# Kernel optimization log

Measured on AMD Instinct MI355X. Metric: run time of the kernel, lower is better.

## Reference

```python
import jax, jax.numpy as jnp
import numpy as np

N, TO, TI, H = 8, 2048, 2048, 128
MASK_FILL = -99999.0  # module uses -99999.0, not -inf


def setup_inputs() -> dict:
    key = jax.random.key(0)
    kq, kv, km = jax.random.split(key, 3)
    queries = jax.random.normal(kq, (N, TO, H), dtype=jnp.float32)
    values = jax.random.normal(kv, (N, TI, H), dtype=jnp.float32)
    # mask is applied to scores.view(-1, Ti) -> shape (N*To, Ti), True = masked
    mask = jax.random.randint(km, (N * TO, TI), 0, 2).astype(bool)
    return {"queries": queries, "values": values, "mask": mask}


def reference(queries, values, mask):
    n, to, h = queries.shape
    ti = values.shape[1]
    # N x To x Ti scores (no 1/sqrt(H) scaling in the original)
    scores = jnp.einsum("nth,nsh->nts", queries, values)
    scores = jnp.where(mask.reshape(n, to, ti), MASK_FILL, scores)
    attention_distribution = jax.nn.softmax(scores, axis=-1)
    attention_output = jnp.einsum("nts,nsh->nth", attention_distribution, values)
    return attention_output, attention_distribution
```

## Files before the change

### kernel.cpp

```cpp
#include <hip/hip_runtime.h>

#define NB  8
#define TOQ 2048
#define TIV 2048
#define HD  128

typedef float f32x4 __attribute__((ext_vector_type(4)));
typedef short s16x8 __attribute__((ext_vector_type(8)));
typedef unsigned short ushort4v __attribute__((ext_vector_type(4)));
typedef unsigned short ushort8v __attribute__((ext_vector_type(8)));

__device__ __forceinline__ unsigned short f2bf(float f) {
    unsigned u = __float_as_uint(f);
    return (unsigned short)((u + 0x7FFFu + ((u >> 16) & 1u)) >> 16);
}
__device__ __forceinline__ float bf2f(unsigned short h) {
    return __uint_as_float(((unsigned)h) << 16);
}

__device__ __forceinline__ void split8(const float4 a, const float4 b,
                                       ushort8v& h, ushort8v& l) {
    const float x[8] = {a.x, a.y, a.z, a.w, b.x, b.y, b.z, b.w};
    #pragma unroll
    for (int j = 0; j < 8; ++j) {
        const unsigned short hi = f2bf(x[j]);
        h[j] = hi;
        l[j] = f2bf(x[j] - bf2f(hi));
    }
}

__device__ __forceinline__ void gload16(const void* g, void* l) {
    __builtin_amdgcn_global_load_lds(
        (const __attribute__((address_space(1))) void*)g,
        (__attribute__((address_space(3))) void*)l, 16, 0, 0);
}

__global__ __launch_bounds__(256) void k0_split(
    const float* __restrict__ Q, const float* __restrict__ V,
    unsigned short* __restrict__ Qh, unsigned short* __restrict__ Ql,
    unsigned short* __restrict__ Vh, unsigned short* __restrict__ Vl)
{
    const size_t i = ((size_t)blockIdx.x * 256 + threadIdx.x) * 8;
    const float* src = blockIdx.y ? V : Q;
    unsigned short* dh = blockIdx.y ? Vh : Qh;
    unsigned short* dl = blockIdx.y ? Vl : Ql;
    const float4 a = *(const float4*)&src[i];
    const float4 b = *(const float4*)&src[i + 4];
    ushort8v h, l;
    split8(a, b, h, l);
    *(ushort8v*)&dh[i] = h;
    *(ushort8v*)&dl[i] = l;
}

__global__ __launch_bounds__(256) void k0_vtf(
    const float* __restrict__ V, unsigned short* __restrict__ VTf)
{
    __shared__ unsigned short tile[64][68];
    const int n  = blockIdx.z;
    const int s0 = blockIdx.x * 64;
    const int h0 = blockIdx.y * 64;
    const int t  = threadIdx.x;

    #pragma unroll
    for (int it = 0; it < 4; ++it) {
        const int f = t + it * 256;
        const int r = f >> 4;
        const int c = f & 15;
        const float4 v = *(const float4*)&V[((size_t)(n * TIV + s0 + r)) * HD + h0 + 4 * c];
        tile[4 * c + 0][r] = f2bf(v.x);
        tile[4 * c + 1][r] = f2bf(v.y);
        tile[4 * c + 2][r] = f2bf(v.z);
        tile[4 * c + 3][r] = f2bf(v.w);
    }
    __syncthreads();

    #pragma unroll
    for (int it = 0; it < 2; ++it) {
        const int s    = t * 2 + it;
        const int k32i = s >> 8;
        const int fni  = (s >> 6) & 3;
        const int l    = s & 63;
        const int hh   = fni * 16 + (l & 15);
        const int kloc = k32i * 32 + ((l >> 4) * 8);
        ushort8v o;
        #pragma unroll
        for (int j = 0; j < 8; ++j) o[j] = tile[hh][kloc + j];
        const size_t k32g = (size_t)(s0 >> 5) + k32i;
        const size_t fng  = (size_t)(h0 >> 4) + fni;
        *(ushort8v*)&VTf[(((size_t)n * 64 + k32g) * 8 + fng) * 512 + (size_t)l * 8] = o;
    }
}

__global__ __launch_bounds__(256) void k0_vt_old(
    const float* __restrict__ V, unsigned short* __restrict__ VT)
{
    __shared__ unsigned short tile[64][68];
    const int n  = blockIdx.z;
    const int s0 = blockIdx.x * 64;
    const int h0 = blockIdx.y * 64;
    const int t  = threadIdx.x;

    #pragma unroll
    for (int it = 0; it < 4; ++it) {
        const int f = t + it * 256;
        const int r = f >> 4;
        const int c = f & 15;
        const float4 v = *(const float4*)&V[((size_t)(n * TIV + s0 + r)) * HD + h0 + 4 * c];
        tile[4 * c + 0][r] = f2bf(v.x);
        tile[4 * c + 1][r] = f2bf(v.y);
        tile[4 * c + 2][r] = f2bf(v.z);
        tile[4 * c + 3][r] = f2bf(v.w);
    }
    __syncthreads();

    #pragma unroll
    for (int it = 0; it < 2; ++it) {
        const int f  = t + it * 256;
        const int hh = f >> 3;
        const int sc = f & 7;
        ushort8v o;
        #pragma unroll
        for (int j = 0; j < 8; ++j) o[j] = tile[hh][8 * sc + j];
        *(ushort8v*)&VT[((size_t)(n * HD + h0 + hh)) * TIV + s0 + 8 * sc] = o;
    }
}

__global__ __launch_bounds__(512) void k1_w8(
    const unsigned short* __restrict__ QhG, const unsigned short* __restrict__ QlG,
    const unsigned short* __restrict__ VhG, const unsigned short* __restrict__ VlG,
    const int* __restrict__ M, unsigned short* __restrict__ Eb,
    float* __restrict__ part)
{
    __shared__ unsigned short qh_l[128 * 32], ql_l[128 * 32];
    __shared__ unsigned short vh_l[128 * 32], vl_l[128 * 32];

    const int n    = blockIdx.z;
    const int tt   = blockIdx.y * 128;
    const int ts   = blockIdx.x * 128;
    const int t    = threadIdx.x;
    const int lane = t & 63;
    const int wave = t >> 6;
    const int wr   = wave >> 2;
    const int wc   = wave & 3;
    const int lr   = lane & 15;
    const int kg   = lane >> 4;

    f32x4 acc[4][2];
    #pragma unroll
    for (int i = 0; i < 4; ++i)
        #pragma unroll
        for (int j = 0; j < 2; ++j) acc[i][j] = (f32x4)0.f;

    for (int h0 = 0; h0 < HD; h0 += 32) {
        {
            const int c   = wave * 64 + lane;
            const int row = c >> 2;
            const int kb  = (c & 3) * 8;
            const int lb  = wave * 512;
            const size_t qo = ((size_t)(n * TOQ + tt + row)) * HD + h0 + kb;
            const size_t vo = ((size_t)(n * TIV + ts + row)) * HD + h0 + kb;
            gload16(QhG + qo, qh_l + lb);
            gload16(QlG + qo, ql_l + lb);
            gload16(VhG + vo, vh_l + lb);
            gload16(VlG + vo, vl_l + lb);
        }
        __syncthreads();

        s16x8 aH[4], aL[4];
        #pragma unroll
        for (int fm = 0; fm < 4; ++fm) {
            const int off = (wr * 64 + fm * 16 + lr) * 32 + kg * 8;
            aH[fm] = *(const s16x8*)(vh_l + off);
            aL[fm] = *(const s16x8*)(vl_l + off);
        }
        #pragma unroll
        for (int fn = 0; fn < 2; ++fn) {
            const int off = (wc * 32 + fn * 16 + lr) * 32 + kg * 8;
            const s16x8 bH = *(const s16x8*)(qh_l + off);
            const s16x8 bL = *(const s16x8*)(ql_l + off);
            #pragma unroll
            for (int fm = 0; fm < 4; ++fm) {
                acc[fm][fn] = __builtin_amdgcn_mfma_f32_16x16x32_bf16(aH[fm], bH, acc[fm][fn], 0, 0, 0);
                acc[fm][fn] = __builtin_amdgcn_mfma_f32_16x16x32_bf16(aH[fm], bL, acc[fm][fn], 0, 0, 0);
                acc[fm][fn] = __builtin_amdgcn_mfma_f32_16x16x32_bf16(aL[fm], bH, acc[fm][fn], 0, 0, 0);
            }
        }
        __syncthreads();
    }

    #pragma unroll
    for (int fn = 0; fn < 2; ++fn) {
        const int to_g = tt + wc * 32 + fn * 16 + lr;
        const size_t rowbase = ((size_t)n * TOQ + to_g) * TIV;
        float rs = 0.f;
        #pragma unroll
        for (int fm = 0; fm < 4; ++fm) {
            const int ti_g = ts + wr * 64 + fm * 16 + kg * 4;
            const int4 mv = *(const int4*)&M[rowbase + ti_g];
            float4 e;
            e.x = mv.x ? 0.f : __expf(acc[fm][fn][0]);
            e.y = mv.y ? 0.f : __expf(acc[fm][fn][1]);
            e.z = mv.z ? 0.f : __expf(acc[fm][fn][2]);
            e.w = mv.w ? 0.f : __expf(acc[fm][fn][3]);
            ushort4v eb;
            eb[0] = f2bf(e.x); eb[1] = f2bf(e.y);
            eb[2] = f2bf(e.z); eb[3] = f2bf(e.w);
            *(ushort4v*)&Eb[rowbase + ti_g] = eb;
            rs += (e.x + e.y) + (e.z + e.w);
        }
        rs += __shfl_xor(rs, 16, 64);
        rs += __shfl_xor(rs, 32, 64);
        if (kg == 0)
            part[((size_t)n * TOQ + to_g) * 32 + blockIdx.x * 2 + wr] = rs;
    }
}

__global__ __launch_bounds__(256) void k1_reg(
    const float* __restrict__ Q, const float* __restrict__ V,
    const int* __restrict__ M, float* __restrict__ E,
    float* __restrict__ part)
{
    __shared__ unsigned short qhi[128 * 32], qlo[128 * 32];
    __shared__ unsigned short vhi[128 * 32], vlo[128 * 32];

    const int n    = blockIdx.z;
    const int tt   = blockIdx.y * 128;
    const int ts   = blockIdx.x * 128;
    const int t    = threadIdx.x;
    const int lane = t & 63;
    const int wave = t >> 6;
    const int wr   = wave >> 1;
    const int wc   = wave & 1;
    const int lr   = lane & 15;
    const int kg   = lane >> 4;

    const float* Qb = Q + ((size_t)n * TOQ + tt) * HD;
    const float* Vb = V + ((size_t)n * TIV + ts) * HD;

    f32x4 acc[4][4];
    #pragma unroll
    for (int i = 0; i < 4; ++i)
        #pragma unroll
        for (int j = 0; j < 4; ++j) acc[i][j] = (f32x4)0.f;

    for (int h0 = 0; h0 < HD; h0 += 32) {
        #pragma unroll
        for (int it = 0; it < 2; ++it) {
            const int i   = t + it * 256;
            const int row = i >> 2;
            const int kb  = i & 3;
            const float* qs = Qb + (size_t)row * HD + h0 + kb * 8;
            const float* vs = Vb + (size_t)row * HD + h0 + kb * 8;
            const float4 q0 = *(const float4*)qs, q1 = *(const float4*)(qs + 4);
            const float4 v0 = *(const float4*)vs, v1 = *(const float4*)(vs + 4);
            ushort8v qh, ql, vh, vl;
            split8(q0, q1, qh, ql);
            split8(v0, v1, vh, vl);
            *(ushort8v*)(qhi + i * 8) = qh;
            *(ushort8v*)(qlo + i * 8) = ql;
            *(ushort8v*)(vhi + i * 8) = vh;
            *(ushort8v*)(vlo + i * 8) = vl;
        }
        __syncthreads();

        s16x8 aH[4], aL[4];
        #pragma unroll
        for (int fm = 0; fm < 4; ++fm) {
            const int off = (wr * 64 + fm * 16 + lr) * 32 + kg * 8;
            aH[fm] = *(const s16x8*)(vhi + off);
            aL[fm] = *(const s16x8*)(vlo + off);
        }
        #pragma unroll
        for (int fn = 0; fn < 4; ++fn) {
            const int off = (wc * 64 + fn * 16 + lr) * 32 + kg * 8;
            const s16x8 bH = *(const s16x8*)(qhi + off);
            const s16x8 bL = *(const s16x8*)(qlo + off);
            #pragma unroll
            for (int fm = 0; fm < 4; ++fm) {
                acc[fm][fn] = __builtin_amdgcn_mfma_f32_16x16x32_bf16(aH[fm], bH, acc[fm][fn], 0, 0, 0);
                acc[fm][fn] = __builtin_amdgcn_mfma_f32_16x16x32_bf16(aH[fm], bL, acc[fm][fn], 0, 0, 0);
                acc[fm][fn] = __builtin_amdgcn_mfma_f32_16x16x32_bf16(aL[fm], bH, acc[fm][fn], 0, 0, 0);
            }
        }
        __syncthreads();
    }

    #pragma unroll
    for (int fn = 0; fn < 4; ++fn) {
        const int to_g = tt + wc * 64 + fn * 16 + lr;
        const size_t rowbase = ((size_t)n * TOQ + to_g) * TIV;
        float rs = 0.f;
        #pragma unroll
        for (int fm = 0; fm < 4; ++fm) {
            const int ti_g = ts + wr * 64 + fm * 16 + kg * 4;
            const int4 mv = *(const int4*)&M[rowbase + ti_g];
            float4 e;
            e.x = mv.x ? 0.f : __expf(acc[fm][fn][0]);
            e.y = mv.y ? 0.f : __expf(acc[fm][fn][1]);
            e.z = mv.z ? 0.f : __expf(acc[fm][fn][2]);
            e.w = mv.w ? 0.f : __expf(acc[fm][fn][3]);
            *(float4*)&E[rowbase + ti_g] = e;
            rs += (e.x + e.y) + (e.z + e.w);
        }
        rs += __shfl_xor(rs, 16, 64);
        rs += __shfl_xor(rs, 32, 64);
        if (kg == 0)
            part[((size_t)n * TOQ + to_g) * 32 + blockIdx.x * 2 + wr] = rs;
    }
}

__global__ __launch_bounds__(256) void k2_rowsum(
    const float* __restrict__ part, float* __restrict__ rec)
{
    const int row = blockIdx.x * 256 + threadIdx.x;
    const float4* p4 = (const float4*)(part + (size_t)row * 32);
    float s = 0.f;
    #pragma unroll
    for (int i = 0; i < 8; ++i) {
        const float4 v = p4[i];
        s += (v.x + v.y) + (v.z + v.w);
    }
    rec[row] = 1.f / s;
}

__global__ __launch_bounds__(512) void k3_pf(
    const unsigned short* __restrict__ Eb, const unsigned short* __restrict__ VTf,
    const float* __restrict__ rec, float* __restrict__ P, float* __restrict__ O)
{
    __shared__ __attribute__((aligned(16))) char smem[50688];
    unsigned short* stg = (unsigned short*)smem;
    float*          red = (float*)smem;

    const int n    = blockIdx.y;
    const int r0   = blockIdx.x * 32;
    const int t    = threadIdx.x;
    const int wave = t >> 6;
    const int lane = t & 63;
    const int p    = wave >> 2;
    const int q    = wave & 3;
    const int lr   = lane & 15;
    const int kg   = lane >> 4;

    const size_t rowbase0 = (size_t)n * TOQ + r0 + p * 16;
    unsigned short* wstg = stg + wave * (16 * 136);

    float rv[4];
    #pragma unroll
    for (int r = 0; r < 4; ++r) rv[r] = rec[rowbase0 + 4 * r + kg];

    f32x4 acc[8];
    #pragma unroll
    for (int fn = 0; fn < 8; ++fn) acc[fn] = (f32x4)0.f;

    const unsigned short* VTn = VTf + (size_t)n * 64 * 8 * 512;

    ushort8v ev[4];
    #pragma unroll
    for (int r = 0; r < 4; ++r)
        ev[r] = *(const ushort8v*)&Eb[(rowbase0 + 4 * r + kg) * TIV + q * 512 + lr * 8];

    for (int kb = 0; kb < 4; ++kb) {
        const int kwin = q * 512 + kb * 128;

        #pragma unroll
        for (int r = 0; r < 4; ++r) {
            const int row_l = 4 * r + kg;
            float pv[8];
            #pragma unroll
            for (int j = 0; j < 8; ++j) pv[j] = bf2f(ev[r][j]) * rv[r];
            float4 p0, p1;
            p0.x = pv[0]; p0.y = pv[1]; p0.z = pv[2]; p0.w = pv[3];
            p1.x = pv[4]; p1.y = pv[5]; p1.z = pv[6]; p1.w = pv[7];
            float* Prow = P + (rowbase0 + row_l) * TIV + kwin + lr * 8;
            *(float4*)Prow       = p0;
            *(float4*)(Prow + 4) = p1;
            ushort8v s8;
            #pragma unroll
            for (int j = 0; j < 8; ++j) s8[j] = f2bf(pv[j]);
            *(ushort8v*)&wstg[row_l * 136 + lr * 8] = s8;
        }

        if (kb < 3) {
            #pragma unroll
            for (int r = 0; r < 4; ++r)
                ev[r] = *(const ushort8v*)&Eb[(rowbase0 + 4 * r + kg) * TIV + kwin + 128 + lr * 8];
        }

        #pragma unroll
        for (int ks = 0; ks < 4; ++ks) {
            const s16x8 a = *(const s16x8*)&wstg[lr * 136 + ks * 32 + kg * 8];
            const int k32 = q * 16 + kb * 4 + ks;
            const unsigned short* bbase = VTn + ((size_t)k32 * 8) * 512 + (size_t)lane * 8;
            #pragma unroll
            for (int fn = 0; fn < 8; ++fn) {
                const s16x8 b = *(const s16x8*)(bbase + (size_t)fn * 512);
                acc[fn] = __builtin_amdgcn_mfma_f32_16x16x32_bf16(a, b, acc[fn], 0, 0, 0);
            }
        }
    }

    __syncthreads();
    if (q != 0) {
        #pragma unroll
        for (int fn = 0; fn < 8; ++fn)
            #pragma unroll
            for (int ri = 0; ri < 4; ++ri)
                red[(((size_t)p * 3 + (q - 1)) * 16 + kg * 4 + ri) * 132 + fn * 16 + lr] = acc[fn][ri];
    }
    __syncthreads();
    if (q == 0) {
        #pragma unroll
        for (int fn = 0; fn < 8; ++fn) {
            #pragma unroll
            for (int ri = 0; ri < 4; ++ri) {
                const int orow = r0 + p * 16 + kg * 4 + ri;
                float o = acc[fn][ri];
                o += red[(((size_t)p * 3 + 0) * 16 + kg * 4 + ri) * 132 + fn * 16 + lr];
                o += red[(((size_t)p * 3 + 1) * 16 + kg * 4 + ri) * 132 + fn * 16 + lr];
                o += red[(((size_t)p * 3 + 2) * 16 + kg * 4 + ri) * 132 + fn * 16 + lr];
                O[((size_t)n * TOQ + orow) * HD + fn * 16 + lr] = o;
            }
        }
    }
}

__global__ __launch_bounds__(512) void k3_pv_old(
    float* __restrict__ EP, const unsigned short* __restrict__ VT,
    const float* __restrict__ rec, float* __restrict__ O)
{
    __shared__ float red[2][3][16][132];

    const int n    = blockIdx.y;
    const int r0   = blockIdx.x * 32;
    const int t    = threadIdx.x;
    const int wave = t >> 6;
    const int lane = t & 63;
    const int p    = wave >> 2;
    const int q    = wave & 3;
    const int lr   = lane & 15;
    const int kg   = lane >> 4;

    const int rowg = r0 + p * 16 + lr;
    const float rc = rec[n * TOQ + rowg];
    float* Erow = EP + ((size_t)n * TOQ + rowg) * TIV;
    const unsigned short* VTb = VT + (size_t)n * HD * TIV;

    f32x4 acc[8];
    #pragma unroll
    for (int fn = 0; fn < 8; ++fn) acc[fn] = (f32x4)0.f;

    const int kbase = q * 512 + kg * 8;

    #pragma unroll 2
    for (int k0 = 0; k0 < 512; k0 += 32) {
        const int k = kbase + k0;
        const float4 e0 = *(const float4*)&Erow[k];
        const float4 e1 = *(const float4*)&Erow[k + 4];
        float4 p0, p1;
        p0.x = e0.x * rc; p0.y = e0.y * rc; p0.z = e0.z * rc; p0.w = e0.w * rc;
        p1.x = e1.x * rc; p1.y = e1.y * rc; p1.z = e1.z * rc; p1.w = e1.w * rc;
        *(float4*)&Erow[k]     = p0;
        *(float4*)&Erow[k + 4] = p1;

        s16x8 a;
        a[0] = (short)f2bf(p0.x); a[1] = (short)f2bf(p0.y);
        a[2] = (short)f2bf(p0.z); a[3] = (short)f2bf(p0.w);
        a[4] = (short)f2bf(p1.x); a[5] = (short)f2bf(p1.y);
        a[6] = (short)f2bf(p1.z); a[7] = (short)f2bf(p1.w);

        #pragma unroll
        for (int fn = 0; fn < 8; ++fn) {
            const s16x8 b = *(const s16x8*)&VTb[(size_t)(fn * 16 + lr) * TIV + k];
            acc[fn] = __builtin_amdgcn_mfma_f32_16x16x32_bf16(a, b, acc[fn], 0, 0, 0);
        }
    }

    if (q != 0) {
        #pragma unroll
        for (int fn = 0; fn < 8; ++fn)
            #pragma unroll
            for (int ri = 0; ri < 4; ++ri)
                red[p][q - 1][kg * 4 + ri][fn * 16 + lr] = acc[fn][ri];
    }
    __syncthreads();
    if (q == 0) {
        #pragma unroll
        for (int fn = 0; fn < 8; ++fn) {
            #pragma unroll
            for (int ri = 0; ri < 4; ++ri) {
                const int orow = r0 + p * 16 + kg * 4 + ri;
                float o = acc[fn][ri];
                o += red[p][0][kg * 4 + ri][fn * 16 + lr];
                o += red[p][1][kg * 4 + ri][fn * 16 + lr];
                o += red[p][2][kg * 4 + ri][fn * 16 + lr];
                O[((size_t)n * TOQ + orow) * HD + fn * 16 + lr] = o;
            }
        }
    }
}

extern "C" void kernel_launch(void* const* d_in, const int* in_sizes, int n_in,
                              void* d_out, int out_size, void* d_ws, size_t ws_size,
                              hipStream_t stream)
{
    const float* Q = (const float*)d_in[0];
    const float* V = (const float*)d_in[1];
    const int*   M = (const int*)d_in[2];

    float* O = (float*)d_out;
    float* P = O + (size_t)NB * TOQ * HD;

    char* ws = (char*)d_ws;
    const size_t partB  = (size_t)NB * TOQ * 32 * 4;
    const size_t vtB    = (size_t)NB * 64 * 8 * 512 * 2;
    const size_t elems  = (size_t)NB * TOQ * HD;
    const size_t sbytes = elems * 2;
    const size_t ebB    = (size_t)NB * TOQ * TIV * 2;

    float*          recb = (float*)ws;
    float*          part = (float*)(ws + (1 << 16));
    unsigned short* VT   = (unsigned short*)(ws + (1 << 16) + partB);
    const size_t splitOff = (1 << 16) + partB + vtB;
    const size_t ebOff    = splitOff + 4 * sbytes;
    const size_t need2    = ebOff + ebB;

    if (ws_size >= need2) {
        unsigned short* Qh = (unsigned short*)(ws + splitOff);
        unsigned short* Ql = (unsigned short*)(ws + splitOff + sbytes);
        unsigned short* Vh = (unsigned short*)(ws + splitOff + 2 * sbytes);
        unsigned short* Vl = (unsigned short*)(ws + splitOff + 3 * sbytes);
        unsigned short* Eb = (unsigned short*)(ws + ebOff);
        k0_vtf  <<<dim3(TIV / 64, HD / 64, NB), 256, 0, stream>>>(V, VT);
        k0_split<<<dim3((unsigned)(elems / 8 / 256), 2), 256, 0, stream>>>(Q, V, Qh, Ql, Vh, Vl);
        k1_w8   <<<dim3(TIV / 128, TOQ / 128, NB), 512, 0, stream>>>(Qh, Ql, Vh, Vl, M, Eb, part);
        k2_rowsum<<<dim3(NB * TOQ / 256), 256, 0, stream>>>(part, recb);
        k3_pf   <<<dim3(TOQ / 32, NB), 512, 0, stream>>>(Eb, VT, recb, P, O);
    } else {
        k0_vt_old<<<dim3(TIV / 64, HD / 64, NB), 256, 0, stream>>>(V, VT);
        k1_reg  <<<dim3(TIV / 128, TOQ / 128, NB), 256, 0, stream>>>(Q, V, M, P, part);
        k2_rowsum<<<dim3(NB * TOQ / 256), 256, 0, stream>>>(part, recb);
        k3_pv_old<<<dim3(TOQ / 32, NB), 512, 0, stream>>>(P, VT, recb, O);
    }
}
```

Measured before the change: 181.8 us.

## Restructure P·V kernel: 16 rows per block, 8-way K split, tree reduction

Replaces the fragment-layout V transpose and the LDS-staged P·V kernel with a kernel that handles 16 query rows per block across 8 waves. Each wave covers a 256-wide K slice, reads E directly from global memory and loads B straight from a plain row-major transposed V. Partial sums are combined with a staged tree reduction through a smaller LDS buffer. The aim is higher occupancy and more blocks, using less LDS and no staging. The cost is strided, less coalesced B loads, extra syncs, and V being reread by twice as many blocks.

```diff
diff --git a/kernel.cpp b/kernel.cpp
--- a/kernel.cpp
+++ b/kernel.cpp
@@ -52,46 +52,7 @@
     *(ushort8v*)&dl[i] = l;
 }
 
-__global__ __launch_bounds__(256) void k0_vtf(
-    const float* __restrict__ V, unsigned short* __restrict__ VTf)
-{
-    __shared__ unsigned short tile[64][68];
-    const int n  = blockIdx.z;
-    const int s0 = blockIdx.x * 64;
-    const int h0 = blockIdx.y * 64;
-    const int t  = threadIdx.x;
-
-    #pragma unroll
-    for (int it = 0; it < 4; ++it) {
-        const int f = t + it * 256;
-        const int r = f >> 4;
-        const int c = f & 15;
-        const float4 v = *(const float4*)&V[((size_t)(n * TIV + s0 + r)) * HD + h0 + 4 * c];
-        tile[4 * c + 0][r] = f2bf(v.x);
-        tile[4 * c + 1][r] = f2bf(v.y);
-        tile[4 * c + 2][r] = f2bf(v.z);
-        tile[4 * c + 3][r] = f2bf(v.w);
-    }
-    __syncthreads();
-
-    #pragma unroll
-    for (int it = 0; it < 2; ++it) {
-        const int s    = t * 2 + it;
-        const int k32i = s >> 8;
-        const int fni  = (s >> 6) & 3;
-        const int l    = s & 63;
-        const int hh   = fni * 16 + (l & 15);
-        const int kloc = k32i * 32 + ((l >> 4) * 8);
-        ushort8v o;
-        #pragma unroll
-        for (int j = 0; j < 8; ++j) o[j] = tile[hh][kloc + j];
-        const size_t k32g = (size_t)(s0 >> 5) + k32i;
-        const size_t fng  = (size_t)(h0 >> 4) + fni;
-        *(ushort8v*)&VTf[(((size_t)n * 64 + k32g) * 8 + fng) * 512 + (size_t)l * 8] = o;
-    }
-}
-
-__global__ __launch_bounds__(256) void k0_vt_old(
+__global__ __launch_bounds__(256) void k0_vt(
     const float* __restrict__ V, unsigned short* __restrict__ VT)
 {
     __shared__ unsigned short tile[64][68];
@@ -323,105 +284,89 @@
     rec[row] = 1.f / s;
 }
 
-__global__ __launch_bounds__(512) void k3_pf(
-    const unsigned short* __restrict__ Eb, const unsigned short* __restrict__ VTf,
+__global__ __launch_bounds__(512) void k3_occ(
+    const unsigned short* __restrict__ Eb, const unsigned short* __restrict__ VT,
     const float* __restrict__ rec, float* __restrict__ P, float* __restrict__ O)
 {
-    __shared__ __attribute__((aligned(16))) char smem[50688];
-    unsigned short* stg = (unsigned short*)smem;
-    float*          red = (float*)smem;
+    __shared__ float red[4][16][132];
 
     const int n    = blockIdx.y;
-    const int r0   = blockIdx.x * 32;
+    const int r0   = blockIdx.x * 16;
     const int t    = threadIdx.x;
-    const int wave = t >> 6;
+    const int q    = t >> 6;
     const int lane = t & 63;
-    const int p    = wave >> 2;
-    const int q    = wave & 3;
     const int lr   = lane & 15;
     const int kg   = lane >> 4;
 
-    const size_t rowbase0 = (size_t)n * TOQ + r0 + p * 16;
-    unsigned short* wstg = stg + wave * (16 * 136);
-
-    float rv[4];
-    #pragma unroll
-    for (int r = 0; r < 4; ++r) rv[r] = rec[rowbase0 + 4 * r + kg];
+    const int rowg = r0 + lr;
+    const float rc = rec[n * TOQ + rowg];
+    const unsigned short* Erow = Eb + ((size_t)n * TOQ + rowg) * TIV;
+    float* Prow = P + ((size_t)n * TOQ + rowg) * TIV;
+    const unsigned short* VTb = VT + (size_t)n * HD * TIV;
 
     f32x4 acc[8];
     #pragma unroll
     for (int fn = 0; fn < 8; ++fn) acc[fn] = (f32x4)0.f;
 
-    const unsigned short* VTn = VTf + (size_t)n * 64 * 8 * 512;
-
-    ushort8v ev[4];
-    #pragma unroll
-    for (int r = 0; r < 4; ++r)
-        ev[r] = *(const ushort8v*)&Eb[(rowbase0 + 4 * r + kg) * TIV + q * 512 + lr * 8];
-
-    for (int kb = 0; kb < 4; ++kb) {
-        const int kwin = q * 512 + kb * 128;
-
-        #pragma unroll
-        for (int r = 0; r < 4; ++r) {
-            const int row_l = 4 * r + kg;
-            float pv[8];
-            #pragma unroll
-            for (int j = 0; j < 8; ++j) pv[j] = bf2f(ev[r][j]) * rv[r];
-            float4 p0, p1;
-            p0.x = pv[0]; p0.y = pv[1]; p0.z = pv[2]; p0.w = pv[3];
-            p1.x = pv[4]; p1.y = pv[5]; p1.z = pv[6]; p1.w = pv[7];
-            float* Prow = P + (rowbase0 + row_l) * TIV + kwin + lr * 8;
-            *(float4*)Prow       = p0;
-            *(float4*)(Prow + 4) = p1;
-            ushort8v s8;
-            #pragma unroll
-            for (int j = 0; j < 8; ++j) s8[j] = f2bf(pv[j]);
-            *(ushort8v*)&wstg[row_l * 136 + lr * 8] = s8;
-        }
-
-        if (kb < 3) {
-            #pragma unroll
-            for (int r = 0; r < 4; ++r)
-                ev[r] = *(const ushort8v*)&Eb[(rowbase0 + 4 * r + kg) * TIV + kwin + 128 + lr * 8];
-        }
-
-        #pragma unroll
-        for (int ks = 0; ks < 4; ++ks) {
-            const s16x8 a = *(const s16x8*)&wstg[lr * 136 + ks * 32 + kg * 8];
-            const int k32 = q * 16 + kb * 4 + ks;
-            const unsigned short* bbase = VTn + ((size_t)k32 * 8) * 512 + (size_t)lane * 8;
-            #pragma unroll
-            for (int fn = 0; fn < 8; ++fn) {
-                const s16x8 b = *(const s16x8*)(bbase + (size_t)fn * 512);
-                acc[fn] = __builtin_amdgcn_mfma_f32_16x16x32_bf16(a, b, acc[fn], 0, 0, 0);
-            }
-        }
-    }
-
-    __syncthreads();
-    if (q != 0) {
-        #pragma unroll
-        for (int fn = 0; fn < 8; ++fn)
-            #pragma unroll
-            for (int ri = 0; ri < 4; ++ri)
-                red[(((size_t)p * 3 + (q - 1)) * 16 + kg * 4 + ri) * 132 + fn * 16 + lr] = acc[fn][ri];
-    }
+    const int kbase = q * 256 + kg * 8;
+
+    #pragma unroll 2
+    for (int k0 = 0; k0 < 256; k0 += 32) {
+        const int k = kbase + k0;
+        const ushort8v ev = *(const ushort8v*)&Erow[k];
+        float pv[8];
+        #pragma unroll
+        for (int j = 0; j < 8; ++j) pv[j] = bf2f(ev[j]) * rc;
+
+        float4 p0, p1;
+        p0.x = pv[0]; p0.y = pv[1]; p0.z = pv[2]; p0.w = pv[3];
+        p1.x = pv[4]; p1.y = pv[5]; p1.z = pv[6]; p1.w = pv[7];
+        *(float4*)&Prow[k]     = p0;
+        *(float4*)&Prow[k + 4] = p1;
+
+        s16x8 a;
+        #pragma unroll
+        for (int j = 0; j < 8; ++j) a[j] = (short)f2bf(pv[j]);
+
+        #pragma unroll
+        for (int fn = 0; fn < 8; ++fn) {
+            const s16x8 b = *(const s16x8*)&VTb[(size_t)(fn * 16 + lr) * TIV + k];
+            acc[fn] = __builtin_amdgcn_mfma_f32_16x16x32_bf16(a, b, acc[fn], 0, 0, 0);
+        }
+    }
+
+    #define PARK(slot)                                                         \
+        _Pragma("unroll") for (int fn = 0; fn < 8; ++fn)                       \
+        _Pragma("unroll") for (int ri = 0; ri < 4; ++ri)                       \
+            red[slot][kg * 4 + ri][fn * 16 + lr] = acc[fn][ri];
+    #define GATHER(slot)                                                       \
+        _Pragma("unroll") for (int fn = 0; fn < 8; ++fn)                       \
+        _Pragma("unroll") for (int ri = 0; ri < 4; ++ri)                       \
+            acc[fn][ri] += red[slot][kg * 4 + ri][fn * 16 + lr];
+
+    if (q & 1) { PARK(q >> 1) }
+    __syncthreads();
+    if (!(q & 1)) { GATHER(q >> 1) }
+    __syncthreads();
+    if (!(q & 1) && (q & 2)) { PARK(q >> 2) }
+    __syncthreads();
+    if (!(q & 3)) { GATHER(q >> 2) }
+    __syncthreads();
+    if (q == 4) { PARK(0) }
     __syncthreads();
     if (q == 0) {
+        GATHER(0)
         #pragma unroll
         for (int fn = 0; fn < 8; ++fn) {
             #pragma unroll
             for (int ri = 0; ri < 4; ++ri) {
-                const int orow = r0 + p * 16 + kg * 4 + ri;
-                float o = acc[fn][ri];
-                o += red[(((size_t)p * 3 + 0) * 16 + kg * 4 + ri) * 132 + fn * 16 + lr];
-                o += red[(((size_t)p * 3 + 1) * 16 + kg * 4 + ri) * 132 + fn * 16 + lr];
-                o += red[(((size_t)p * 3 + 2) * 16 + kg * 4 + ri) * 132 + fn * 16 + lr];
-                O[((size_t)n * TOQ + orow) * HD + fn * 16 + lr] = o;
+                const int orow = r0 + kg * 4 + ri;
+                O[((size_t)n * TOQ + orow) * HD + fn * 16 + lr] = acc[fn][ri];
             }
         }
     }
+    #undef PARK
+    #undef GATHER
 }
 
 __global__ __launch_bounds__(512) void k3_pv_old(
@@ -512,7 +457,7 @@
 
     char* ws = (char*)d_ws;
     const size_t partB  = (size_t)NB * TOQ * 32 * 4;
-    const size_t vtB    = (size_t)NB * 64 * 8 * 512 * 2;
+    const size_t vtB    = (size_t)NB * HD * TIV * 2;
     const size_t elems  = (size_t)NB * TOQ * HD;
     const size_t sbytes = elems * 2;
     const size_t ebB    = (size_t)NB * TOQ * TIV * 2;
@@ -524,19 +469,19 @@
     const size_t ebOff    = splitOff + 4 * sbytes;
     const size_t need2    = ebOff + ebB;
 
+    k0_vt<<<dim3(TIV / 64, HD / 64, NB), 256, 0, stream>>>(V, VT);
+
     if (ws_size >= need2) {
         unsigned short* Qh = (unsigned short*)(ws + splitOff);
         unsigned short* Ql = (unsigned short*)(ws + splitOff + sbytes);
         unsigned short* Vh = (unsigned short*)(ws + splitOff + 2 * sbytes);
         unsigned short* Vl = (unsigned short*)(ws + splitOff + 3 * sbytes);
         unsigned short* Eb = (unsigned short*)(ws + ebOff);
-        k0_vtf  <<<dim3(TIV / 64, HD / 64, NB), 256, 0, stream>>>(V, VT);
         k0_split<<<dim3((unsigned)(elems / 8 / 256), 2), 256, 0, stream>>>(Q, V, Qh, Ql, Vh, Vl);
         k1_w8   <<<dim3(TIV / 128, TOQ / 128, NB), 512, 0, stream>>>(Qh, Ql, Vh, Vl, M, Eb, part);
         k2_rowsum<<<dim3(NB * TOQ / 256), 256, 0, stream>>>(part, recb);
-        k3_pf   <<<dim3(TOQ / 32, NB), 512, 0, stream>>>(Eb, VT, recb, P, O);
+        k3_occ  <<<dim3(TOQ / 16, NB), 512, 0, stream>>>(Eb, VT, recb, P, O);
     } else {
-        k0_vt_old<<<dim3(TIV / 64, HD / 64, NB), 256, 0, stream>>>(V, VT);
         k1_reg  <<<dim3(TIV / 128, TOQ / 128, NB), 256, 0, stream>>>(Q, V, M, P, part);
         k2_rowsum<<<dim3(NB * TOQ / 256), 256, 0, stream>>>(part, recb);
         k3_pv_old<<<dim3(TOQ / 32, NB), 512, 0, stream>>>(P, VT, recb, O);
```

Result: faster. 176.2 us, median of 2 (-3.1%).
